# Optimization experiments

Measured on AMD Instinct MI355X. Metric: run time of the kernel, lower is better.

The kernel has to match this reference:

```python
import jax, jax.numpy as jnp
import numpy as np

IN_FEATURES = 512
OUT_FEATURES = 512
BATCH = 1024
MU_INIT = 0.0
LOGVAR_INIT = -5.0


def setup_inputs() -> dict:
    key = jax.random.key(0)
    k_x, k_ew, k_eb, k_wm, k_wl, k_bm, k_bl = jax.random.split(key, 7)
    x = jax.random.normal(k_x, (BATCH, IN_FEATURES), dtype=jnp.float32)
    eps_w = jax.random.normal(k_ew, (BATCH, OUT_FEATURES, IN_FEATURES), dtype=jnp.float32)
    eps_b = jax.random.normal(k_eb, (BATCH, OUT_FEATURES), dtype=jnp.float32)
    weight_mu = MU_INIT + 0.1 * jax.random.normal(k_wm, (OUT_FEATURES, IN_FEATURES), dtype=jnp.float32)
    weight_logvar = LOGVAR_INIT + 0.1 * jax.random.normal(k_wl, (OUT_FEATURES, IN_FEATURES), dtype=jnp.float32)
    bias_mu = MU_INIT + 0.1 * jax.random.normal(k_bm, (OUT_FEATURES,), dtype=jnp.float32)
    bias_logvar = LOGVAR_INIT + 0.1 * jax.random.normal(k_bl, (OUT_FEATURES,), dtype=jnp.float32)
    return {
        "x": x, "eps_w": eps_w, "eps_b": eps_b,
        "weight_mu": weight_mu, "weight_logvar": weight_logvar,
        "bias_mu": bias_mu, "bias_logvar": bias_logvar,
    }


def reference(x, eps_w, eps_b, weight_mu, weight_logvar, bias_mu, bias_logvar):
    # Per-sample reparameterized weights: W_b = mu + exp(0.5*logvar) * eps_b
    weight_std = jnp.exp(0.5 * weight_logvar)          # (O, I)
    bias_std = jnp.exp(0.5 * bias_logvar)              # (O,)
    weights = weight_mu[None] + weight_std[None] * eps_w   # (B, O, I)
    biases = bias_mu[None] + bias_std[None] * eps_b        # (B, O)
    # Batched matvec: out[b,o] = sum_i W[b,o,i] * x[b,i]
    out = jnp.einsum("boi,bi->bo", weights, x) + biases
    return out
```

## Files before the change

kernel.cpp:

```cpp
#include <hip/hip_runtime.h>
#include <hip/hip_bf16.h>

#define IN_F    512
#define OUT_F   512
#define BATCH_N 1024
#define OCHUNK  32
#define NB      4

typedef float f32x4 __attribute__((ext_vector_type(4)));

__global__ __launch_bounds__(256) void std_precompute_kernel(
    const float* __restrict__ wlv, const float* __restrict__ blv,
    float* __restrict__ wstd, float* __restrict__ bstd)
{
    int i = blockIdx.x * blockDim.x + threadIdx.x;
    f32x4 v = reinterpret_cast<const f32x4*>(wlv)[i];
    f32x4 s;
    s.x = expf(0.5f * v.x);
    s.y = expf(0.5f * v.y);
    s.z = expf(0.5f * v.z);
    s.w = expf(0.5f * v.w);
    reinterpret_cast<f32x4*>(wstd)[i] = s;
    if (blockIdx.x == 0 && threadIdx.x < OUT_F / 4) {
        f32x4 bv = reinterpret_cast<const f32x4*>(blv)[threadIdx.x];
        f32x4 bs;
        bs.x = expf(0.5f * bv.x);
        bs.y = expf(0.5f * bv.y);
        bs.z = expf(0.5f * bv.z);
        bs.w = expf(0.5f * bv.w);
        reinterpret_cast<f32x4*>(bstd)[threadIdx.x] = bs;
    }
}

template <bool STD_IN_WS>
__global__ __launch_bounds__(256) void bayes_main_kernel(
    const float* __restrict__ x,
    const float* __restrict__ eps_w,
    const float* __restrict__ eps_b,
    const float* __restrict__ wmu,
    const float* __restrict__ wstd_or_lv,
    const float* __restrict__ bmu,
    const float* __restrict__ bstd_or_lv,
    float* __restrict__ out)
{
    const int wid  = threadIdx.x >> 6;
    const int lane = threadIdx.x & 63;
    const int c    = blockIdx.x & 15;
    const int bq   = blockIdx.x >> 4;
    const int b0   = bq * 16 + wid * NB;
    const int o0   = c * OCHUNK;

    f32x4 xa[NB], xb[NB];
    #pragma unroll
    for (int ib = 0; ib < NB; ++ib) {
        const float* xp = x + (size_t)(b0 + ib) * IN_F;
        xa[ib] = *reinterpret_cast<const f32x4*>(xp + lane * 4);
        xb[ib] = *reinterpret_cast<const f32x4*>(xp + 256 + lane * 4);
    }

    #pragma unroll 1
    for (int oo = 0; oo < OCHUNK; ++oo) {
        const int o = o0 + oo;

        f32x4 ea[NB], eb[NB];
        #pragma unroll
        for (int ib = 0; ib < NB; ++ib) {
            const f32x4* ep = reinterpret_cast<const f32x4*>(
                eps_w + ((size_t)(b0 + ib) * OUT_F + o) * IN_F);
            ea[ib] = __builtin_nontemporal_load(ep + lane);
            eb[ib] = __builtin_nontemporal_load(ep + 64 + lane);
        }

        const f32x4 ma = *reinterpret_cast<const f32x4*>(wmu + (size_t)o * IN_F + lane * 4);
        const f32x4 mb = *reinterpret_cast<const f32x4*>(wmu + (size_t)o * IN_F + 256 + lane * 4);
        f32x4 sa = *reinterpret_cast<const f32x4*>(wstd_or_lv + (size_t)o * IN_F + lane * 4);
        f32x4 sb = *reinterpret_cast<const f32x4*>(wstd_or_lv + (size_t)o * IN_F + 256 + lane * 4);
        if (!STD_IN_WS) {
            sa.x = expf(0.5f * sa.x); sa.y = expf(0.5f * sa.y);
            sa.z = expf(0.5f * sa.z); sa.w = expf(0.5f * sa.w);
            sb.x = expf(0.5f * sb.x); sb.y = expf(0.5f * sb.y);
            sb.z = expf(0.5f * sb.z); sb.w = expf(0.5f * sb.w);
        }

        float acc[NB];
        #pragma unroll
        for (int ib = 0; ib < NB; ++ib) {
            float a;
            a = fmaf(sa.x, ea[ib].x, ma.x) * xa[ib].x;
            a = fmaf(fmaf(sa.y, ea[ib].y, ma.y), xa[ib].y, a);
            a = fmaf(fmaf(sa.z, ea[ib].z, ma.z), xa[ib].z, a);
            a = fmaf(fmaf(sa.w, ea[ib].w, ma.w), xa[ib].w, a);
            a = fmaf(fmaf(sb.x, eb[ib].x, mb.x), xb[ib].x, a);
            a = fmaf(fmaf(sb.y, eb[ib].y, mb.y), xb[ib].y, a);
            a = fmaf(fmaf(sb.z, eb[ib].z, mb.z), xb[ib].z, a);
            a = fmaf(fmaf(sb.w, eb[ib].w, mb.w), xb[ib].w, a);
            acc[ib] = a;
        }

        #pragma unroll
        for (int off = 32; off >= 1; off >>= 1) {
            #pragma unroll
            for (int ib = 0; ib < NB; ++ib)
                acc[ib] += __shfl_xor(acc[ib], off, 64);
        }

        if (lane == 0) {
            const float bm = bmu[o];
            float bs = bstd_or_lv[o];
            if (!STD_IN_WS) bs = expf(0.5f * bs);
            #pragma unroll
            for (int ib = 0; ib < NB; ++ib) {
                const float ebv = __builtin_nontemporal_load(
                    eps_b + (size_t)(b0 + ib) * OUT_F + o);
                out[(size_t)(b0 + ib) * OUT_F + o] = acc[ib] + bm + bs * ebv;
            }
        }
    }
}

extern "C" void kernel_launch(void* const* d_in, const int* in_sizes, int n_in,
                              void* d_out, int out_size, void* d_ws, size_t ws_size,
                              hipStream_t stream) {
    const float* x      = (const float*)d_in[0];
    const float* eps_w  = (const float*)d_in[1];
    const float* eps_b  = (const float*)d_in[2];
    const float* wmu    = (const float*)d_in[3];
    const float* wlv    = (const float*)d_in[4];
    const float* bmu    = (const float*)d_in[5];
    const float* blv    = (const float*)d_in[6];
    float* out = (float*)d_out;

    const int blocks = (BATCH_N / (4 * NB)) * (OUT_F / OCHUNK);

    const size_t std_bytes = (size_t)OUT_F * IN_F * sizeof(float) + OUT_F * sizeof(float);
    if (ws_size >= std_bytes) {
        float* wstd = (float*)d_ws;
        float* bstd = wstd + (size_t)OUT_F * IN_F;
        std_precompute_kernel<<<OUT_F * IN_F / 4 / 256, 256, 0, stream>>>(wlv, blv, wstd, bstd);
        bayes_main_kernel<true><<<blocks, 256, 0, stream>>>(
            x, eps_w, eps_b, wmu, wstd, bmu, bstd, out);
    } else {
        bayes_main_kernel<false><<<blocks, 256, 0, stream>>>(
            x, eps_w, eps_b, wmu, wlv, bmu, blv, out);
    }
}
```

Baseline: 196.8 us.

## Split batch into two launches mixing nontemporal and cached eps loads

```diff
diff --git a/kernel.cpp b/kernel.cpp
--- a/kernel.cpp
+++ b/kernel.cpp
@@ -4,7 +4,7 @@
 #define IN_F    512
 #define OUT_F   512
 #define BATCH_N 1024
-#define OCHUNK  32
+#define OCHUNK  16
 #define NB      4
 
 typedef float f32x4 __attribute__((ext_vector_type(4)));
@@ -32,22 +32,23 @@
     }
 }
 
-template <bool STD_IN_WS>
+template <bool NT>
 __global__ __launch_bounds__(256) void bayes_main_kernel(
     const float* __restrict__ x,
     const float* __restrict__ eps_w,
     const float* __restrict__ eps_b,
     const float* __restrict__ wmu,
-    const float* __restrict__ wstd_or_lv,
+    const float* __restrict__ wstd,
     const float* __restrict__ bmu,
-    const float* __restrict__ bstd_or_lv,
-    float* __restrict__ out)
+    const float* __restrict__ bstd,
+    float* __restrict__ out,
+    int b_base)
 {
     const int wid  = threadIdx.x >> 6;
     const int lane = threadIdx.x & 63;
-    const int c    = blockIdx.x & 15;
-    const int bq   = blockIdx.x >> 4;
-    const int b0   = bq * 16 + wid * NB;
+    const int c    = blockIdx.x & 31;
+    const int bq   = blockIdx.x >> 5;
+    const int b0   = b_base + bq * 16 + wid * NB;
     const int o0   = c * OCHUNK;
 
     f32x4 xa[NB], xb[NB];
@@ -58,6 +59,8 @@
         xb[ib] = *reinterpret_cast<const f32x4*>(xp + 256 + lane * 4);
     }
 
+    const int q = lane >> 4;
+
     #pragma unroll 1
     for (int oo = 0; oo < OCHUNK; ++oo) {
         const int o = o0 + oo;
@@ -67,20 +70,19 @@
         for (int ib = 0; ib < NB; ++ib) {
             const f32x4* ep = reinterpret_cast<const f32x4*>(
                 eps_w + ((size_t)(b0 + ib) * OUT_F + o) * IN_F);
-            ea[ib] = __builtin_nontemporal_load(ep + lane);
-            eb[ib] = __builtin_nontemporal_load(ep + 64 + lane);
+            if (NT) {
+                ea[ib] = __builtin_nontemporal_load(ep + lane);
+                eb[ib] = __builtin_nontemporal_load(ep + 64 + lane);
+            } else {
+                ea[ib] = ep[lane];
+                eb[ib] = ep[64 + lane];
+            }
         }
 
         const f32x4 ma = *reinterpret_cast<const f32x4*>(wmu + (size_t)o * IN_F + lane * 4);
         const f32x4 mb = *reinterpret_cast<const f32x4*>(wmu + (size_t)o * IN_F + 256 + lane * 4);
-        f32x4 sa = *reinterpret_cast<const f32x4*>(wstd_or_lv + (size_t)o * IN_F + lane * 4);
-        f32x4 sb = *reinterpret_cast<const f32x4*>(wstd_or_lv + (size_t)o * IN_F + 256 + lane * 4);
-        if (!STD_IN_WS) {
-            sa.x = expf(0.5f * sa.x); sa.y = expf(0.5f * sa.y);
-            sa.z = expf(0.5f * sa.z); sa.w = expf(0.5f * sa.w);
-            sb.x = expf(0.5f * sb.x); sb.y = expf(0.5f * sb.y);
-            sb.z = expf(0.5f * sb.z); sb.w = expf(0.5f * sb.w);
-        }
+        const f32x4 sa = *reinterpret_cast<const f32x4*>(wstd + (size_t)o * IN_F + lane * 4);
+        const f32x4 sb = *reinterpret_cast<const f32x4*>(wstd + (size_t)o * IN_F + 256 + lane * 4);
 
         float acc[NB];
         #pragma unroll
@@ -98,22 +100,95 @@
         }
 
         #pragma unroll
-        for (int off = 32; off >= 1; off >>= 1) {
-            #pragma unroll
-            for (int ib = 0; ib < NB; ++ib)
-                acc[ib] += __shfl_xor(acc[ib], off, 64);
-        }
-
-        if (lane == 0) {
-            const float bm = bmu[o];
-            float bs = bstd_or_lv[o];
-            if (!STD_IN_WS) bs = expf(0.5f * bs);
-            #pragma unroll
-            for (int ib = 0; ib < NB; ++ib) {
-                const float ebv = __builtin_nontemporal_load(
-                    eps_b + (size_t)(b0 + ib) * OUT_F + o);
-                out[(size_t)(b0 + ib) * OUT_F + o] = acc[ib] + bm + bs * ebv;
-            }
+        for (int ib = 0; ib < NB; ++ib) {
+            acc[ib] += __shfl_xor(acc[ib], 32, 64);
+            acc[ib] += __shfl_xor(acc[ib], 16, 64);
+        }
+        float v = q == 0 ? acc[0] : (q == 1 ? acc[1] : (q == 2 ? acc[2] : acc[3]));
+        v += __shfl_xor(v, 8, 64);
+        v += __shfl_xor(v, 4, 64);
+        v += __shfl_xor(v, 2, 64);
+        v += __shfl_xor(v, 1, 64);
+
+        if ((lane & 15) == 0) {
+            const size_t oidx = (size_t)(b0 + q) * OUT_F + o;
+            float ebv;
+            if (NT) ebv = __builtin_nontemporal_load(eps_b + oidx);
+            else    ebv = eps_b[oidx];
+            out[oidx] = v + bmu[o] + bstd[o] * ebv;
+        }
+    }
+}
+
+__global__ __launch_bounds__(256) void bayes_fallback_kernel(
+    const float* __restrict__ x, const float* __restrict__ eps_w,
+    const float* __restrict__ eps_b, const float* __restrict__ wmu,
+    const float* __restrict__ wlv, const float* __restrict__ bmu,
+    const float* __restrict__ blv, float* __restrict__ out, int b_base)
+{
+    const int wid  = threadIdx.x >> 6;
+    const int lane = threadIdx.x & 63;
+    const int c    = blockIdx.x & 31;
+    const int bq   = blockIdx.x >> 5;
+    const int b0   = b_base + bq * 16 + wid * NB;
+    const int o0   = c * OCHUNK;
+
+    f32x4 xa[NB], xb[NB];
+    #pragma unroll
+    for (int ib = 0; ib < NB; ++ib) {
+        const float* xp = x + (size_t)(b0 + ib) * IN_F;
+        xa[ib] = *reinterpret_cast<const f32x4*>(xp + lane * 4);
+        xb[ib] = *reinterpret_cast<const f32x4*>(xp + 256 + lane * 4);
+    }
+    const int q = lane >> 4;
+
+    #pragma unroll 1
+    for (int oo = 0; oo < OCHUNK; ++oo) {
+        const int o = o0 + oo;
+        f32x4 ea[NB], eb[NB];
+        #pragma unroll
+        for (int ib = 0; ib < NB; ++ib) {
+            const f32x4* ep = reinterpret_cast<const f32x4*>(
+                eps_w + ((size_t)(b0 + ib) * OUT_F + o) * IN_F);
+            ea[ib] = ep[lane];
+            eb[ib] = ep[64 + lane];
+        }
+        const f32x4 ma = *reinterpret_cast<const f32x4*>(wmu + (size_t)o * IN_F + lane * 4);
+        const f32x4 mb = *reinterpret_cast<const f32x4*>(wmu + (size_t)o * IN_F + 256 + lane * 4);
+        f32x4 sa = *reinterpret_cast<const f32x4*>(wlv + (size_t)o * IN_F + lane * 4);
+        f32x4 sb = *reinterpret_cast<const f32x4*>(wlv + (size_t)o * IN_F + 256 + lane * 4);
+        sa.x = expf(0.5f * sa.x); sa.y = expf(0.5f * sa.y);
+        sa.z = expf(0.5f * sa.z); sa.w = expf(0.5f * sa.w);
+        sb.x = expf(0.5f * sb.x); sb.y = expf(0.5f * sb.y);
+        sb.z = expf(0.5f * sb.z); sb.w = expf(0.5f * sb.w);
+
+        float acc[NB];
+        #pragma unroll
+        for (int ib = 0; ib < NB; ++ib) {
+            float a;
+            a = fmaf(sa.x, ea[ib].x, ma.x) * xa[ib].x;
+            a = fmaf(fmaf(sa.y, ea[ib].y, ma.y), xa[ib].y, a);
+            a = fmaf(fmaf(sa.z, ea[ib].z, ma.z), xa[ib].z, a);
+            a = fmaf(fmaf(sa.w, ea[ib].w, ma.w), xa[ib].w, a);
+            a = fmaf(fmaf(sb.x, eb[ib].x, mb.x), xb[ib].x, a);
+            a = fmaf(fmaf(sb.y, eb[ib].y, mb.y), xb[ib].y, a);
+            a = fmaf(fmaf(sb.z, eb[ib].z, mb.z), xb[ib].z, a);
+            a = fmaf(fmaf(sb.w, eb[ib].w, mb.w), xb[ib].w, a);
+            acc[ib] = a;
+        }
+        #pragma unroll
+        for (int ib = 0; ib < NB; ++ib) {
+            acc[ib] += __shfl_xor(acc[ib], 32, 64);
+            acc[ib] += __shfl_xor(acc[ib], 16, 64);
+        }
+        float v = q == 0 ? acc[0] : (q == 1 ? acc[1] : (q == 2 ? acc[2] : acc[3]));
+        v += __shfl_xor(v, 8, 64);
+        v += __shfl_xor(v, 4, 64);
+        v += __shfl_xor(v, 2, 64);
+        v += __shfl_xor(v, 1, 64);
+        if ((lane & 15) == 0) {
+            const size_t oidx = (size_t)(b0 + q) * OUT_F + o;
+            out[oidx] = v + bmu[o] + expf(0.5f * blv[o]) * eps_b[oidx];
         }
     }
 }
@@ -130,7 +205,7 @@
     const float* blv    = (const float*)d_in[6];
     float* out = (float*)d_out;
 
-    const int blocks = (BATCH_N / (4 * NB)) * (OUT_F / OCHUNK);
+    const int blocks = (BATCH_N / 2 / (4 * NB)) * (OUT_F / OCHUNK);
 
     const size_t std_bytes = (size_t)OUT_F * IN_F * sizeof(float) + OUT_F * sizeof(float);
     if (ws_size >= std_bytes) {
@@ -138,9 +213,13 @@
         float* bstd = wstd + (size_t)OUT_F * IN_F;
         std_precompute_kernel<<<OUT_F * IN_F / 4 / 256, 256, 0, stream>>>(wlv, blv, wstd, bstd);
         bayes_main_kernel<true><<<blocks, 256, 0, stream>>>(
-            x, eps_w, eps_b, wmu, wstd, bmu, bstd, out);
+            x, eps_w, eps_b, wmu, wstd, bmu, bstd, out, 0);
+        bayes_main_kernel<false><<<blocks, 256, 0, stream>>>(
+            x, eps_w, eps_b, wmu, wstd, bmu, bstd, out, BATCH_N / 2);
     } else {
-        bayes_main_kernel<false><<<blocks, 256, 0, stream>>>(
-            x, eps_w, eps_b, wmu, wlv, bmu, blv, out);
-    }
-}
+        bayes_fallback_kernel<<<blocks, 256, 0, stream>>>(
+            x, eps_w, eps_b, wmu, wlv, bmu, blv, out, 0);
+        bayes_fallback_kernel<<<blocks, 256, 0, stream>>>(
+            x, eps_w, eps_b, wmu, wlv, bmu, blv, out, BATCH_N / 2);
+    }
+}
```

Measured after the change: 223.8 us. 13.7% more time.
